# Kernel optimization log

Hardware: AMD Instinct MI355X
Metric: run time of the kernel (lower is better)

## Reference

```python
import jax, jax.numpy as jnp
import numpy as np
import math

B, T, E, H = 4, 1024, 1024, 16
HD = E // H  # 64, even -> rope_dim == head_dim, no pass-through
SCALE = HD ** -0.5
PI = math.pi


def setup_inputs() -> dict:
    key = jax.random.key(0)
    ks = jax.random.split(key, 16)
    d = {}
    d["x_real"] = jax.random.normal(ks[0], (B, T, E), jnp.float32)
    d["x_imag"] = jax.random.normal(ks[1], (B, T, E), jnp.float32)
    d["lat"] = jax.random.uniform(ks[2], (B, T), jnp.float32) * 180.0
    d["lon"] = jax.random.uniform(ks[3], (B, T), jnp.float32) * 360.0
    i = 4
    for p in ("q", "k", "v", "o"):
        d[p + "_log_mag"] = jax.random.normal(ks[i], (E, E), jnp.float32) * 0.1; i += 1
        d[p + "_phase"] = jax.random.uniform(ks[i], (E, E), jnp.float32, minval=-PI, maxval=PI); i += 1
        d[p + "_bmag"] = jnp.zeros((E,), jnp.float32)
        d[p + "_bphase"] = jnp.zeros((E,), jnp.float32)
    d["dist_scale"] = jax.random.normal(ks[i], (H,), jnp.float32) * 0.1 - 0.5; i += 1
    d["dist_offset"] = jnp.zeros((H,), jnp.float32)
    return d


def _clinear(xr, xi, log_mag, phase, bmag, bphase):
    # Complex linear with magnitude-phase weights: W = exp(log_mag) * e^{i*phase}
    mag = jnp.exp(log_mag)
    wr = mag * jnp.cos(phase)
    wi = mag * jnp.sin(phase)
    r = xr @ wr.T - xi @ wi.T + bmag * jnp.cos(bphase)
    im = xr @ wi.T + xi @ wr.T + bmag * jnp.sin(bphase)
    return r, im


def _rotate_half(x):
    x1, x2 = jnp.split(x, 2, axis=-1)
    return jnp.concatenate([-x2, x1], axis=-1)


def _rope(xr, xi, cos_full, sin_full):
    # applied identically to real and imag parts (head_dim even -> full rope)
    r = xr * cos_full + _rotate_half(xr) * sin_full
    im = xi * cos_full + _rotate_half(xi) * sin_full
    return r, im


def _heads(x):  # [B,T,E] -> [B,H,T,HD]
    return x.reshape(B, T, H, HD).transpose(0, 2, 1, 3)


def _forward(x_real, x_imag, lat, lon,
             q_log_mag, q_phase, q_bmag, q_bphase,
             k_log_mag, k_phase, k_bmag, k_bphase,
             v_log_mag, v_phase, v_bmag, v_bphase,
             o_log_mag, o_phase, o_bmag, o_bphase,
             dist_scale, dist_offset):
    qr, qi = _clinear(x_real, x_imag, q_log_mag, q_phase, q_bmag, q_bphase)
    kr, ki = _clinear(x_real, x_imag, k_log_mag, k_phase, k_bmag, k_bphase)
    vr, vi = _clinear(x_real, x_imag, v_log_mag, v_phase, v_bmag, v_bphase)
    qr, qi, kr, ki, vr, vi = map(_heads, (qr, qi, kr, ki, vr, vi))

    # complex RoPE cache
    pos = jnp.arange(T, dtype=jnp.float32)
    inv_freq = 1.0 / (10000.0 ** (jnp.arange(0, HD, 2, dtype=jnp.float32) / HD))
    freqs = pos[:, None] * inv_freq[None, :]          # [T, HD/2]
    cos = jnp.cos(freqs); sin = jnp.sin(freqs)
    cos_full = jnp.concatenate([cos, cos], -1)[None, None]  # [1,1,T,HD]
    sin_full = jnp.concatenate([sin, sin], -1)[None, None]
    qr, qi = _rope(qr, qi, cos_full, sin_full)
    kr, ki = _rope(kr, ki, cos_full, sin_full)

    # Hermitian attention scores: Re(Q K^H) = Re(Q)Re(K)^T + Im(Q)Im(K)^T
    scores = (jnp.einsum('bhqd,bhkd->bhqk', qr, kr)
              + jnp.einsum('bhqd,bhkd->bhqk', qi, ki)) * SCALE

    # spatial attention bias via haversine distance
    lat_rad = (lat - 90.0) / 180.0 * PI
    lon_rad = lon / 360.0 * (2.0 * PI)
    lat1 = lat_rad[:, :, None]; lat2 = lat_rad[:, None, :]   # [B,T,1],[B,1,T]
    dlat = lat2 - lat1
    dlon = lon_rad[:, None, :] - lon_rad[:, :, None]
    a = jnp.sin(dlat / 2) ** 2 + jnp.cos(lat1) * jnp.cos(lat2) * jnp.sin(dlon / 2) ** 2
    dist_deg = 2.0 * jnp.arcsin(jnp.sqrt(jnp.clip(a, 0.0, 1.0))) * (180.0 / PI)
    log_dist = jnp.log1p(dist_deg)[:, None]                  # [B,1,T,T]
    bias = dist_scale[None, :, None, None] * log_dist + dist_offset[None, :, None, None]
    scores = scores + bias

    # causal mask (block_size == T)
    causal = jnp.tril(jnp.ones((T, T), dtype=bool))
    scores = jnp.where(causal[None, None], scores, jnp.float32(-1e9))
    attn = jax.nn.softmax(scores, axis=-1)

    # complex value aggregation: real attention weights times complex V
    or_ = jnp.einsum('bhqk,bhkd->bhqd', attn, vr)
    oi_ = jnp.einsum('bhqk,bhkd->bhqd', attn, vi)
    or_ = or_.transpose(0, 2, 1, 3).reshape(B, T, E)
    oi_ = oi_.transpose(0, 2, 1, 3).reshape(B, T, E)

    yr, yi = _clinear(or_, oi_, o_log_mag, o_phase, o_bmag, o_bphase)
    return jnp.stack([yr, yi])  # [2,B,T,E] (real, imag)


def reference(x_real, x_imag, lat, lon,
              q_log_mag, q_phase, q_bmag, q_bphase,
              k_log_mag, k_phase, k_bmag, k_bphase,
              v_log_mag, v_phase, v_bmag, v_bphase,
              o_log_mag, o_phase, o_bmag, o_bphase,
              dist_scale, dist_offset):
    return _forward(x_real, x_imag, lat, lon,
                    q_log_mag, q_phase, q_bmag, q_bphase,
                    k_log_mag, k_phase, k_bmag, k_bphase,
                    v_log_mag, v_phase, v_bmag, v_bphase,
                    o_log_mag, o_phase, o_bmag, o_bphase,
                    dist_scale, dist_offset)
```

## Files before the change

### kernel.cpp

```cpp
#include <hip/hip_runtime.h>
#include <math.h>

#define B_ 4
#define T_ 1024
#define E_ 1024
#define H_ 16
#define HD_ 64

constexpr float SCALE_ = 0.125f;
constexpr float PI_F = 3.14159265358979323846f;

constexpr size_t BTE = (size_t)B_ * T_ * E_;
constexpr size_t BTT = (size_t)B_ * T_ * T_;
constexpr int M_ = B_ * T_;
constexpr int KC_ = 2 * E_;

typedef __attribute__((ext_vector_type(8))) short bf16x8;
typedef __attribute__((ext_vector_type(4))) float f32x4;

__device__ __forceinline__ short f2bf(float f) {
    unsigned int u = __float_as_uint(f);
    unsigned int r = (u + 0x7fffu + ((u >> 16) & 1u)) >> 16;
    return (short)r;
}
__device__ __forceinline__ float bf2f(short s) {
    return __uint_as_float(((unsigned int)(unsigned short)s) << 16);
}
__device__ __forceinline__ void fsplit(float v, short& h, short& l) {
    short hh = f2bf(v);
    h = hh;
    l = f2bf(v - bf2f(hh));
}
__device__ __forceinline__ void gl_lds16(const void* g, void* l) {
    __builtin_amdgcn_global_load_lds(
        (const __attribute__((address_space(1))) unsigned int*)g,
        (__attribute__((address_space(3))) unsigned int*)l, 16, 0, 0);
}

__global__ __launch_bounds__(256) void wgen(const float* __restrict__ lm,
                                            const float* __restrict__ ph,
                                            short* __restrict__ W) {
    int idx = blockIdx.x * 256 + threadIdx.x;
    int n = idx >> 10, k = idx & 1023;
    float m = expf(lm[idx]);
    float s, c;
    sincosf(ph[idx], &s, &c);
    float wr = m * c, wi = m * s;
    size_t r0 = (size_t)n * KC_;
    size_t r1 = (size_t)(n + 1024) * KC_;
    W[r0 + k]        = f2bf(wr);
    W[r0 + 1024 + k] = f2bf(-wi);
    W[r1 + k]        = f2bf(wi);
    W[r1 + 1024 + k] = f2bf(wr);
}

__global__ __launch_bounds__(256) void wgen_split(const float* __restrict__ lm,
                                                  const float* __restrict__ ph,
                                                  short* __restrict__ Wh,
                                                  short* __restrict__ Wl) {
    int idx = blockIdx.x * 256 + threadIdx.x;
    int n = idx >> 10, k = idx & 1023;
    float m = expf(lm[idx]);
    float s, c;
    sincosf(ph[idx], &s, &c);
    float wr = m * c, wi = m * s;
    size_t o0 = (size_t)n * KC_ + k;
    size_t o1 = (size_t)n * KC_ + 1024 + k;
    size_t o2 = (size_t)(n + 1024) * KC_ + k;
    size_t o3 = (size_t)(n + 1024) * KC_ + 1024 + k;
    short h, l;
    fsplit(wr,  h, l); Wh[o0] = h; Wl[o0] = l;
    fsplit(-wi, h, l); Wh[o1] = h; Wl[o1] = l;
    fsplit(wi,  h, l); Wh[o2] = h; Wl[o2] = l;
    fsplit(wr,  h, l); Wh[o3] = h; Wl[o3] = l;
}

__global__ __launch_bounds__(256) void xcat_split(const float* __restrict__ xr,
                                                  const float* __restrict__ xi,
                                                  short* __restrict__ xh,
                                                  short* __restrict__ xl) {
    size_t idx = (size_t)blockIdx.x * 256 + threadIdx.x;
    size_t m = idx >> 10, k = idx & 1023;
    short h, l;
    fsplit(xr[idx], h, l);
    xh[m * KC_ + k] = h; xl[m * KC_ + k] = l;
    fsplit(xi[idx], h, l);
    xh[m * KC_ + 1024 + k] = h; xl[m * KC_ + 1024 + k] = l;
}

__global__ __launch_bounds__(256) void geodist(const float* __restrict__ lat,
                                               const float* __restrict__ lon,
                                               short* __restrict__ ld) {
    size_t idx = (size_t)blockIdx.x * 256 + threadIdx.x;
    int k = (int)(idx & (T_ - 1));
    int q = (int)((idx >> 10) & (T_ - 1));
    int b = (int)(idx >> 20);
    float la1 = (lat[b * T_ + q] - 90.f) * (PI_F / 180.f);
    float la2 = (lat[b * T_ + k] - 90.f) * (PI_F / 180.f);
    float lo1 = lon[b * T_ + q] * (PI_F / 180.f);
    float lo2 = lon[b * T_ + k] * (PI_F / 180.f);
    float sdla = sinf((la2 - la1) * 0.5f);
    float sdlo = sinf((lo2 - lo1) * 0.5f);
    float a = sdla * sdla + cosf(la1) * cosf(la2) * sdlo * sdlo;
    a = fminf(fmaxf(a, 0.f), 1.f);
    float dd = 2.f * asinf(sqrtf(a)) * (180.f / PI_F);
    ld[idx] = f2bf(log1pf(dd));
}

__global__ __launch_bounds__(512, 2) void cgemm_qk2(const short* __restrict__ Ah,
                                                    const short* __restrict__ Al,
                                                    const short* __restrict__ Qwh,
                                                    const short* __restrict__ Qwl,
                                                    const short* __restrict__ Kwh,
                                                    const short* __restrict__ Kwl,
                                                    const float* __restrict__ qbm,
                                                    const float* __restrict__ qbp,
                                                    const float* __restrict__ kbm,
                                                    const float* __restrict__ kbp,
                                                    short* __restrict__ Qh,
                                                    short* __restrict__ Ql,
                                                    short* __restrict__ Kh,
                                                    short* __restrict__ Kl) {
    __shared__ short lds[2][4096 * 8];

    const int tid = threadIdx.x;
    const int w = tid >> 6, l = tid & 63;
    const int wm = w >> 1;
    const int wn = w & 1;
    const int wl = l & 15, g = l >> 4;

    const int id = blockIdx.x;
    const int x = id & 7;
    const int j = id >> 3;
    const int bm = ((x & 3) * 4 + (j & 3)) * 256;
    const int bnc = ((x >> 2) * 8 + (j >> 2)) * 128;

    f32x4 accQ[4][4], accK[4][4];
#pragma unroll
    for (int m = 0; m < 4; ++m)
#pragma unroll
        for (int n = 0; n < 4; ++n) {
            accQ[m][n] = (f32x4){0.f, 0.f, 0.f, 0.f};
            accK[m][n] = (f32x4){0.f, 0.f, 0.f, 0.f};
        }

    auto stage = [&](int k0, int buf) {
#pragma unroll
        for (int i = 0; i < 8; ++i) {
            const int c = i * 512 + tid;
            short* dst = &lds[buf][(size_t)c * 8];
            if (c < 2048) {
                const int row = c >> 3, c8 = (c & 7) ^ (row & 7);
                gl_lds16(((c8 < 4) ? Ah : Al) + (size_t)(bm + row) * KC_ + k0 + (c8 & 3) * 8, dst);
            } else if (c < 3072) {
                const int lc = c - 2048, row = lc >> 3, c8 = (lc & 7) ^ (row & 7);
                gl_lds16(((c8 < 4) ? Qwh : Qwl) + (size_t)(bnc + row) * KC_ + k0 + (c8 & 3) * 8, dst);
            } else {
                const int lc = c - 3072, row = lc >> 3, c8 = (lc & 7) ^ (row & 7);
                gl_lds16(((c8 < 4) ? Kwh : Kwl) + (size_t)(bnc + row) * KC_ + k0 + (c8 & 3) * 8, dst);
            }
        }
    };

    const int NT = KC_ / 32;
    stage(0, 0);
    __syncthreads();

    int cur = 0;
    for (int t = 0; t < NT; ++t) {
        if (t + 1 < NT) stage((t + 1) * 32, cur ^ 1);

        const short* sA = &lds[cur][0];
        const short* sQ = &lds[cur][2048 * 8];
        const short* sK = &lds[cur][3072 * 8];

        bf16x8 afh[4], afl[4];
#pragma unroll
        for (int m = 0; m < 4; ++m) {
            const int ra = wm * 64 + m * 16 + wl;
            const int sw = ra & 7;
            afh[m] = *(const bf16x8*)&sA[(ra * 8 + (g ^ sw)) * 8];
            afl[m] = *(const bf16x8*)&sA[(ra * 8 + ((g + 4) ^ sw)) * 8];
        }
#pragma unroll
        for (int n = 0; n < 4; ++n) {
            const int rb = wn * 64 + n * 16 + wl;
            const int sw = rb & 7;
            const bf16x8 qh_ = *(const bf16x8*)&sQ[(rb * 8 + (g ^ sw)) * 8];
            const bf16x8 ql_ = *(const bf16x8*)&sQ[(rb * 8 + ((g + 4) ^ sw)) * 8];
            const bf16x8 kh_ = *(const bf16x8*)&sK[(rb * 8 + (g ^ sw)) * 8];
            const bf16x8 kl_ = *(const bf16x8*)&sK[(rb * 8 + ((g + 4) ^ sw)) * 8];
#pragma unroll
            for (int m = 0; m < 4; ++m) {
                accQ[m][n] = __builtin_amdgcn_mfma_f32_16x16x32_bf16(afh[m], qh_, accQ[m][n], 0, 0, 0);
                accQ[m][n] = __builtin_amdgcn_mfma_f32_16x16x32_bf16(afh[m], ql_, accQ[m][n], 0, 0, 0);
                accQ[m][n] = __builtin_amdgcn_mfma_f32_16x16x32_bf16(afl[m], qh_, accQ[m][n], 0, 0, 0);
                accK[m][n] = __builtin_amdgcn_mfma_f32_16x16x32_bf16(afh[m], kh_, accK[m][n], 0, 0, 0);
                accK[m][n] = __builtin_amdgcn_mfma_f32_16x16x32_bf16(afh[m], kl_, accK[m][n], 0, 0, 0);
                accK[m][n] = __builtin_amdgcn_mfma_f32_16x16x32_bf16(afl[m], kh_, accK[m][n], 0, 0, 0);
            }
        }
        __syncthreads();
        cur ^= 1;
    }

#pragma unroll
    for (int n = 0; n < 4; ++n) {
        const int col = bnc + wn * 64 + n * 16 + wl;
        const int ch = col & 1023;
        float qs, qc, ks, kc;
        sincosf(qbp[ch], &qs, &qc);
        sincosf(kbp[ch], &ks, &kc);
        const float qbias = qbm[ch] * (col < 1024 ? qc : qs);
        const float kbias = kbm[ch] * (col < 1024 ? kc : ks);
#pragma unroll
        for (int m = 0; m < 4; ++m)
#pragma unroll
            for (int r = 0; r < 4; ++r) {
                accQ[m][n][r] += qbias;
                accK[m][n][r] += kbias;
            }
    }

#pragma unroll
    for (int n = 0; n < 2; ++n) {
        const int jf = n * 16 + wl;
        const float invf = expf(-(2.f * jf / 64.f) * 9.210340371976184f);
#pragma unroll
        for (int m = 0; m < 4; ++m)
#pragma unroll
            for (int r = 0; r < 4; ++r) {
                const int row = bm + wm * 64 + m * 16 + g * 4 + r;
                const float th = (float)(row & 1023) * invf;
                float s_, c_;
                sincosf(th, &s_, &c_);
                float x1 = accQ[m][n][r], x2 = accQ[m][n + 2][r];
                accQ[m][n][r]     = x1 * c_ - x2 * s_;
                accQ[m][n + 2][r] = x2 * c_ + x1 * s_;
                x1 = accK[m][n][r]; x2 = accK[m][n + 2][r];
                accK[m][n][r]     = x1 * c_ - x2 * s_;
                accK[m][n + 2][r] = x2 * c_ + x1 * s_;
            }
    }

#pragma unroll
    for (int n = 0; n < 4; ++n) {
        const int col = bnc + wn * 64 + n * 16 + wl;
        const int ch = col & 1023;
        const int off = (ch >> 6) * 128 + (ch & 63) + ((col >= 1024) ? 64 : 0);
#pragma unroll
        for (int m = 0; m < 4; ++m)
#pragma unroll
            for (int r = 0; r < 4; ++r) {
                const int row = bm + wm * 64 + m * 16 + g * 4 + r;
                short h_, l_;
                fsplit(accQ[m][n][r], h_, l_);
                Qh[(size_t)row * KC_ + off] = h_;
                Ql[(size_t)row * KC_ + off] = l_;
                fsplit(accK[m][n][r], h_, l_);
                Kh[(size_t)row * KC_ + off] = h_;
                Kl[(size_t)row * KC_ + off] = l_;
            }
    }
}

__global__ __launch_bounds__(256) void cgemm_mfma(const short* __restrict__ A,
                                                  const short* __restrict__ W,
                                                  const float* __restrict__ bmag,
                                                  const float* __restrict__ bphase,
                                                  short* __restrict__ outbf,
                                                  float* __restrict__ outr,
                                                  float* __restrict__ outi,
                                                  int mode) {
    __shared__ short lds[2][1024 * 8];

    const int tid = threadIdx.x;
    const int w = tid >> 6, l = tid & 63;
    const int wm = w >> 1, wn = w & 1;
    const int wl = l & 15, g = l >> 4;

    int id = blockIdx.y * 32 + blockIdx.x;
    int swz = (id & 7) * 64 + (id >> 3);
    const int bm = (swz & 31) * 128;
    const int bn = (swz >> 5) * 128;

    f32x4 acc[4][4];
#pragma unroll
    for (int m = 0; m < 4; ++m)
#pragma unroll
        for (int n = 0; n < 4; ++n) acc[m][n] = (f32x4){0.f, 0.f, 0.f, 0.f};

    auto stage = [&](int k0, int buf) {
#pragma unroll
        for (int i = 0; i < 4; ++i) {
            const int c = i * 256 + tid;
            const int row = c >> 3, c8 = (c & 7) ^ (row & 7);
            const short* src = (c8 < 4)
                ? A + (size_t)(bm + row) * KC_ + k0 + (c8 & 3) * 8
                : W + (size_t)(bn + row) * KC_ + k0 + (c8 & 3) * 8;
            gl_lds16(src, &lds[buf][(size_t)c * 8]);
        }
    };

    const int NT = KC_ / 32;
    stage(0, 0);
    __syncthreads();

    int cur = 0;
    for (int t = 0; t < NT; ++t) {
        if (t + 1 < NT) stage((t + 1) * 32, cur ^ 1);

        const short* sAB = lds[cur];
        bf16x8 af[4], bfr[4];
#pragma unroll
        for (int m = 0; m < 4; ++m) {
            const int ra = wm * 64 + m * 16 + wl;
            af[m] = *(const bf16x8*)&sAB[(ra * 8 + (g ^ (ra & 7))) * 8];
        }
#pragma unroll
        for (int n = 0; n < 4; ++n) {
            const int rb = wn * 64 + n * 16 + wl;
            bfr[n] = *(const bf16x8*)&sAB[(rb * 8 + ((g + 4) ^ (rb & 7))) * 8];
        }
#pragma unroll
        for (int m = 0; m < 4; ++m)
#pragma unroll
            for (int n = 0; n < 4; ++n)
                acc[m][n] = __builtin_amdgcn_mfma_f32_16x16x32_bf16(af[m], bfr[n], acc[m][n], 0, 0, 0);

        __syncthreads();
        cur ^= 1;
    }

#pragma unroll
    for (int n = 0; n < 4; ++n) {
        const int col = bn + wn * 64 + n * 16 + wl;
        const int ch = col & 1023;
        float sb, cb;
        sincosf(bphase[ch], &sb, &cb);
        const float bias = bmag[ch] * (col < 1024 ? cb : sb);
#pragma unroll
        for (int m = 0; m < 4; ++m) {
#pragma unroll
            for (int r = 0; r < 4; ++r) {
                const int row = bm + wm * 64 + m * 16 + g * 4 + r;
                const float v = acc[m][n][r] + bias;
                if (mode == 0) {
                    const int hh = ch >> 6, d = ch & 63;
                    outbf[(size_t)row * KC_ + hh * 128 + d + ((col >= 1024) ? 64 : 0)] = f2bf(v);
                } else {
                    if (col < 1024) outr[(size_t)row * E_ + col] = v;
                    else            outi[(size_t)row * E_ + (col - 1024)] = v;
                }
            }
        }
    }
}

__global__ __launch_bounds__(512) void attn_split(const short* __restrict__ qh,
                                                  const short* __restrict__ ql,
                                                  const short* __restrict__ kh,
                                                  const short* __restrict__ kl,
                                                  const short* __restrict__ vc,
                                                  const short* __restrict__ ldb,
                                                  const float* __restrict__ dsc,
                                                  const float* __restrict__ dof,
                                                  short* __restrict__ otc) {
    __shared__ short sKh[64 * 128];
    __shared__ short sKl[64 * 128];
    __shared__ short sV[2][64 * 66];
    __shared__ short sP[8][16 * 68];

    const int j = blockIdx.x;
    const int h = j & 15;
    const int idx = j >> 4;
    const int b = idx & 3;
    const int q4 = idx >> 2;
    const int qt = (q4 < 4) ? (7 - q4) : (q4 - 4);

    const int tid = threadIdx.x;
    const int w = tid >> 6, l = tid & 63;
    const int wl = l & 15, g = l >> 4;

    const float dsch = dsc[h], dofh = dof[h];

    bf16x8 aqh[4], aql[4];
    {
        const size_t qbase = ((size_t)(b * T_) + qt * 128 + w * 16 + wl) * KC_ + h * 128;
#pragma unroll
        for (int ks = 0; ks < 4; ++ks) {
            aqh[ks] = *(const bf16x8*)(qh + qbase + ks * 32 + g * 8);
            aql[ks] = *(const bf16x8*)(ql + qbase + ks * 32 + g * 8);
        }
    }

    f32x4 accR[4], accI[4];
#pragma unroll
    for (int nb = 0; nb < 4; ++nb) {
        accR[nb] = (f32x4){0.f, 0.f, 0.f, 0.f};
        accI[nb] = (f32x4){0.f, 0.f, 0.f, 0.f};
    }
    float m_run[4], l_run[4];
#pragma unroll
    for (int r = 0; r < 4; ++r) { m_run[r] = -3.0e38f; l_run[r] = 0.f; }

    const int nkt = 2 * qt + 2;
    for (int kt = 0; kt < nkt; ++kt) {
        __syncthreads();

#pragma unroll
        for (int i = 0; i < 2; ++i) {
            int chunk = (w * 2 + i) * 64 + l;
            int row = chunk >> 4;
            int c8 = (chunk & 15) ^ (row & 15);
            size_t src = ((size_t)(b * T_) + kt * 64 + row) * KC_ + h * 128 + c8 * 8;
            gl_lds16(kh + src, sKh + (w * 2 + i) * 64 * 8);
            gl_lds16(kl + src, sKl + (w * 2 + i) * 64 * 8);
        }
        {
            const short* vrow = vc + ((size_t)(b * T_) + kt * 64 + l) * KC_ + h * 128;
            const int comp = w >> 2;
            const int d0 = (w & 3) * 16;
#pragma unroll
            for (int half = 0; half < 2; ++half) {
                bf16x8 v8 = *(const bf16x8*)(vrow + comp * 64 + d0 + half * 8);
#pragma unroll
                for (int jj = 0; jj < 8; ++jj) sV[comp][(d0 + half * 8 + jj) * 66 + l] = v8[jj];
            }
        }
        __syncthreads();

        f32x4 s[4];
#pragma unroll
        for (int nb = 0; nb < 4; ++nb) s[nb] = (f32x4){0.f, 0.f, 0.f, 0.f};
#pragma unroll
        for (int nb = 0; nb < 4; ++nb) {
            const int ktl = nb * 16 + wl;
#pragma unroll
            for (int ks = 0; ks < 4; ++ks) {
                const int pc8 = (ks * 4 + g) ^ (ktl & 15);
                const bf16x8 bkh = *(const bf16x8*)&sKh[ktl * 128 + pc8 * 8];
                const bf16x8 bkl = *(const bf16x8*)&sKl[ktl * 128 + pc8 * 8];
                s[nb] = __builtin_amdgcn_mfma_f32_16x16x32_bf16(aqh[ks], bkh, s[nb], 0, 0, 0);
                s[nb] = __builtin_amdgcn_mfma_f32_16x16x32_bf16(aqh[ks], bkl, s[nb], 0, 0, 0);
                s[nb] = __builtin_amdgcn_mfma_f32_16x16x32_bf16(aql[ks], bkh, s[nb], 0, 0, 0);
            }
        }

        const int qg0 = qt * 128 + w * 16 + g * 4;
        const int kg0 = kt * 64;
        const bool domask = (kt >= 2 * qt);
#pragma unroll
        for (int nb = 0; nb < 4; ++nb) {
            const int kg = kg0 + nb * 16 + wl;
            const short* ldp = ldb + ((size_t)b * T_ + qg0) * T_ + kg;
#pragma unroll
            for (int r = 0; r < 4; ++r) {
                float sv = s[nb][r] * SCALE_ + dsch * bf2f(ldp[(size_t)r * T_]) + dofh;
                if (domask && kg > qg0 + r) sv = -1.0e9f;
                s[nb][r] = sv;
            }
        }

#pragma unroll
        for (int r = 0; r < 4; ++r) {
            float mt = fmaxf(fmaxf(s[0][r], s[1][r]), fmaxf(s[2][r], s[3][r]));
            mt = fmaxf(mt, __shfl_xor(mt, 1));
            mt = fmaxf(mt, __shfl_xor(mt, 2));
            mt = fmaxf(mt, __shfl_xor(mt, 4));
            mt = fmaxf(mt, __shfl_xor(mt, 8));
            const float mnew = fmaxf(m_run[r], mt);
            const float sc = __expf(m_run[r] - mnew);
            m_run[r] = mnew;
            float rs = 0.f;
#pragma unroll
            for (int nb = 0; nb < 4; ++nb) {
                const float p = __expf(s[nb][r] - mnew);
                s[nb][r] = p;
                rs += p;
            }
            rs += __shfl_xor(rs, 1);
            rs += __shfl_xor(rs, 2);
            rs += __shfl_xor(rs, 4);
            rs += __shfl_xor(rs, 8);
            l_run[r] = l_run[r] * sc + rs;
#pragma unroll
            for (int nb = 0; nb < 4; ++nb) { accR[nb][r] *= sc; accI[nb][r] *= sc; }
        }

#pragma unroll
        for (int nb = 0; nb < 4; ++nb)
#pragma unroll
            for (int r = 0; r < 4; ++r)
                sP[w][(g * 4 + r) * 68 + nb * 16 + wl] = f2bf(s[nb][r]);

        bf16x8 ap[2];
#pragma unroll
        for (int ks = 0; ks < 2; ++ks)
            ap[ks] = *(const bf16x8*)&sP[w][wl * 68 + ks * 32 + g * 8];
#pragma unroll
        for (int nb = 0; nb < 4; ++nb) {
#pragma unroll
            for (int ks = 0; ks < 2; ++ks) {
                const bf16x8 bvr = *(const bf16x8*)&sV[0][(nb * 16 + wl) * 66 + ks * 32 + g * 8];
                const bf16x8 bvi = *(const bf16x8*)&sV[1][(nb * 16 + wl) * 66 + ks * 32 + g * 8];
                accR[nb] = __builtin_amdgcn_mfma_f32_16x16x32_bf16(ap[ks], bvr, accR[nb], 0, 0, 0);
                accI[nb] = __builtin_amdgcn_mfma_f32_16x16x32_bf16(ap[ks], bvi, accI[nb], 0, 0, 0);
            }
        }
    }

    float inv[4];
#pragma unroll
    for (int r = 0; r < 4; ++r) inv[r] = 1.0f / l_run[r];
#pragma unroll
    for (int nb = 0; nb < 4; ++nb) {
#pragma unroll
        for (int r = 0; r < 4; ++r) {
            const int q = qt * 128 + w * 16 + g * 4 + r;
            const int d = nb * 16 + wl;
            const size_t base = ((size_t)(b * T_) + q) * KC_ + h * 64 + d;
            otc[base] = f2bf(accR[nb][r] * inv[r]);
            otc[base + 1024] = f2bf(accI[nb][r] * inv[r]);
        }
    }
}

extern "C" void kernel_launch(void* const* d_in, const int* in_sizes, int n_in,
                              void* d_out, int out_size, void* d_ws, size_t ws_size,
                              hipStream_t stream) {
    const float* x_r  = (const float*)d_in[0];
    const float* x_i  = (const float*)d_in[1];
    const float* lat  = (const float*)d_in[2];
    const float* lon  = (const float*)d_in[3];
    const float* q_lm = (const float*)d_in[4];
    const float* q_ph = (const float*)d_in[5];
    const float* q_bm = (const float*)d_in[6];
    const float* q_bp = (const float*)d_in[7];
    const float* k_lm = (const float*)d_in[8];
    const float* k_ph = (const float*)d_in[9];
    const float* k_bm = (const float*)d_in[10];
    const float* k_bp = (const float*)d_in[11];
    const float* v_lm = (const float*)d_in[12];
    const float* v_ph = (const float*)d_in[13];
    const float* v_bm = (const float*)d_in[14];
    const float* v_bp = (const float*)d_in[15];
    const float* o_lm = (const float*)d_in[16];
    const float* o_ph = (const float*)d_in[17];
    const float* o_bm = (const float*)d_in[18];
    const float* o_bp = (const float*)d_in[19];
    const float* dsc  = (const float*)d_in[20];
    const float* dof  = (const float*)d_in[21];

    char* ws = (char*)d_ws;
    const size_t MB = 1024u * 1024u;
    short* Wv  = (short*)(ws + 0 * MB);
    short* Wo  = (short*)(ws + 8 * MB);
    short* Wqh = (short*)(ws + 16 * MB);
    short* Wql = (short*)(ws + 24 * MB);
    short* Wkh = (short*)(ws + 32 * MB);
    short* Wkl = (short*)(ws + 40 * MB);
    short* xch = (short*)(ws + 48 * MB);
    short* xcl = (short*)(ws + 64 * MB);
    short* qhh = (short*)(ws + 80 * MB);
    short* qll = (short*)(ws + 96 * MB);
    short* khh = (short*)(ws + 112 * MB);
    short* kll = (short*)(ws + 128 * MB);
    short* vcb = (short*)(ws + 144 * MB);
    short* otc = (short*)(ws + 160 * MB);
    short* ldt = (short*)(ws + 176 * MB);

    wgen_split<<<(E_ * E_) / 256, 256, 0, stream>>>(q_lm, q_ph, Wqh, Wql);
    wgen_split<<<(E_ * E_) / 256, 256, 0, stream>>>(k_lm, k_ph, Wkh, Wkl);
    wgen<<<(E_ * E_) / 256, 256, 0, stream>>>(v_lm, v_ph, Wv);
    wgen<<<(E_ * E_) / 256, 256, 0, stream>>>(o_lm, o_ph, Wo);
    xcat_split<<<BTE / 256, 256, 0, stream>>>(x_r, x_i, xch, xcl);
    geodist<<<BTT / 256, 256, 0, stream>>>(lat, lon, ldt);

    cgemm_qk2<<<256, 512, 0, stream>>>(xch, xcl, Wqh, Wql, Wkh, Wkl,
                                       q_bm, q_bp, k_bm, k_bp,
                                       qhh, qll, khh, kll);

    dim3 ggrid(M_ / 128, KC_ / 128);
    cgemm_mfma<<<ggrid, 256, 0, stream>>>(xch, Wv, v_bm, v_bp, vcb, nullptr, nullptr, 0);

    attn_split<<<512, 512, 0, stream>>>(qhh, qll, khh, kll, vcb, ldt, dsc, dof, otc);

    float* yr = (float*)d_out;
    float* yi = (float*)d_out + BTE;
    cgemm_mfma<<<ggrid, 256, 0, stream>>>(otc, Wo, o_bm, o_bp, nullptr, yr, yi, 1);
}
```

Measured before the change: 603.6 us.

## Deepen GEMM LDS pipeline to two tiles in flight with explicit vmcnt waits

Both GEMM kernels now keep two K-tiles in flight. They replace __syncthreads with raw s_barrier plus explicit s_waitcnt vmcnt/lgkmcnt counts, and load all LDS fragments into registers before a second barrier. The next-next tile is then issued into the just-consumed buffer before the MFMA block runs. This is meant to hide global-to-LDS latency behind compute and avoid the full vmcnt(0) drain that __syncthreads implies. The cost is more fragment registers, and correctness depends on the hardcoded vmcnt counts matching the number of loads each stage issues.

```diff
diff --git a/kernel.cpp b/kernel.cpp
--- a/kernel.cpp
+++ b/kernel.cpp
@@ -35,6 +35,11 @@
     __builtin_amdgcn_global_load_lds(
         (const __attribute__((address_space(1))) unsigned int*)g,
         (__attribute__((address_space(3))) unsigned int*)l, 16, 0, 0);
+}
+__device__ __forceinline__ void barrier_raw() {
+    asm volatile("" ::: "memory");
+    __builtin_amdgcn_s_barrier();
+    asm volatile("" ::: "memory");
 }
 
 __global__ __launch_bounds__(256) void wgen(const float* __restrict__ lm,
@@ -164,17 +169,20 @@
 
     const int NT = KC_ / 32;
     stage(0, 0);
-    __syncthreads();
+    stage(32, 1);
 
     int cur = 0;
     for (int t = 0; t < NT; ++t) {
-        if (t + 1 < NT) stage((t + 1) * 32, cur ^ 1);
+        if (t == NT - 1) asm volatile("s_waitcnt vmcnt(0)" ::: "memory");
+        else             asm volatile("s_waitcnt vmcnt(8)" ::: "memory");
+        __builtin_amdgcn_sched_barrier(0);
+        barrier_raw();
 
         const short* sA = &lds[cur][0];
         const short* sQ = &lds[cur][2048 * 8];
         const short* sK = &lds[cur][3072 * 8];
 
-        bf16x8 afh[4], afl[4];
+        bf16x8 afh[4], afl[4], qh_[4], ql_[4], kh_[4], kl_[4];
 #pragma unroll
         for (int m = 0; m < 4; ++m) {
             const int ra = wm * 64 + m * 16 + wl;
@@ -186,21 +194,29 @@
         for (int n = 0; n < 4; ++n) {
             const int rb = wn * 64 + n * 16 + wl;
             const int sw = rb & 7;
-            const bf16x8 qh_ = *(const bf16x8*)&sQ[(rb * 8 + (g ^ sw)) * 8];
-            const bf16x8 ql_ = *(const bf16x8*)&sQ[(rb * 8 + ((g + 4) ^ sw)) * 8];
-            const bf16x8 kh_ = *(const bf16x8*)&sK[(rb * 8 + (g ^ sw)) * 8];
-            const bf16x8 kl_ = *(const bf16x8*)&sK[(rb * 8 + ((g + 4) ^ sw)) * 8];
+            qh_[n] = *(const bf16x8*)&sQ[(rb * 8 + (g ^ sw)) * 8];
+            ql_[n] = *(const bf16x8*)&sQ[(rb * 8 + ((g + 4) ^ sw)) * 8];
+            kh_[n] = *(const bf16x8*)&sK[(rb * 8 + (g ^ sw)) * 8];
+            kl_[n] = *(const bf16x8*)&sK[(rb * 8 + ((g + 4) ^ sw)) * 8];
+        }
+        asm volatile("s_waitcnt lgkmcnt(0)" ::: "memory");
+        __builtin_amdgcn_sched_barrier(0);
+        barrier_raw();
+
+        if (t + 2 < NT) stage((t + 2) * 32, cur);
+
+#pragma unroll
+        for (int n = 0; n < 4; ++n) {
 #pragma unroll
             for (int m = 0; m < 4; ++m) {
-                accQ[m][n] = __builtin_amdgcn_mfma_f32_16x16x32_bf16(afh[m], qh_, accQ[m][n], 0, 0, 0);
-                accQ[m][n] = __builtin_amdgcn_mfma_f32_16x16x32_bf16(afh[m], ql_, accQ[m][n], 0, 0, 0);
-                accQ[m][n] = __builtin_amdgcn_mfma_f32_16x16x32_bf16(afl[m], qh_, accQ[m][n], 0, 0, 0);
-                accK[m][n] = __builtin_amdgcn_mfma_f32_16x16x32_bf16(afh[m], kh_, accK[m][n], 0, 0, 0);
-                accK[m][n] = __builtin_amdgcn_mfma_f32_16x16x32_bf16(afh[m], kl_, accK[m][n], 0, 0, 0);
-                accK[m][n] = __builtin_amdgcn_mfma_f32_16x16x32_bf16(afl[m], kh_, accK[m][n], 0, 0, 0);
-            }
-        }
-        __syncthreads();
+                accQ[m][n] = __builtin_amdgcn_mfma_f32_16x16x32_bf16(afh[m], qh_[n], accQ[m][n], 0, 0, 0);
+                accQ[m][n] = __builtin_amdgcn_mfma_f32_16x16x32_bf16(afh[m], ql_[n], accQ[m][n], 0, 0, 0);
+                accQ[m][n] = __builtin_amdgcn_mfma_f32_16x16x32_bf16(afl[m], qh_[n], accQ[m][n], 0, 0, 0);
+                accK[m][n] = __builtin_amdgcn_mfma_f32_16x16x32_bf16(afh[m], kh_[n], accK[m][n], 0, 0, 0);
+                accK[m][n] = __builtin_amdgcn_mfma_f32_16x16x32_bf16(afh[m], kl_[n], accK[m][n], 0, 0, 0);
+                accK[m][n] = __builtin_amdgcn_mfma_f32_16x16x32_bf16(afl[m], kh_[n], accK[m][n], 0, 0, 0);
+            }
+        }
         cur ^= 1;
     }
 
@@ -304,11 +320,14 @@
 
     const int NT = KC_ / 32;
     stage(0, 0);
-    __syncthreads();
+    stage(32, 1);
 
     int cur = 0;
     for (int t = 0; t < NT; ++t) {
-        if (t + 1 < NT) stage((t + 1) * 32, cur ^ 1);
+        if (t == NT - 1) asm volatile("s_waitcnt vmcnt(0)" ::: "memory");
+        else             asm volatile("s_waitcnt vmcnt(4)" ::: "memory");
+        __builtin_amdgcn_sched_barrier(0);
+        barrier_raw();
 
         const short* sAB = lds[cur];
         bf16x8 af[4], bfr[4];
@@ -322,13 +341,18 @@
             const int rb = wn * 64 + n * 16 + wl;
             bfr[n] = *(const bf16x8*)&sAB[(rb * 8 + ((g + 4) ^ (rb & 7))) * 8];
         }
+        asm volatile("s_waitcnt lgkmcnt(0)" ::: "memory");
+        __builtin_amdgcn_sched_barrier(0);
+        barrier_raw();
+
+        if (t + 2 < NT) stage((t + 2) * 32, cur);
+
 #pragma unroll
         for (int m = 0; m < 4; ++m)
 #pragma unroll
             for (int n = 0; n < 4; ++n)
                 acc[m][n] = __builtin_amdgcn_mfma_f32_16x16x32_bf16(af[m], bfr[n], acc[m][n], 0, 0, 0);
 
-        __syncthreads();
         cur ^= 1;
     }
 
```

Result: slower. 834.7 us (+38.3%).

## Load QK GEMM A-operand directly to registers and shrink tile to 128 rows

Applied to the files above, without the earlier changes.

The fused Q/K projection GEMM now uses 256-thread blocks with a 128x128 output tile, launched as 512 blocks instead of 256. Activation (A) fragments are prefetched straight from global memory into registers one k-step ahead, so only the Q and K weight tiles are staged through LDS. This halves LDS usage and spreads work over more blocks, at the cost of more register pressure for the prefetched fragments and uncoalesced, unshared global reads of A.

```diff
diff --git a/kernel.cpp b/kernel.cpp
--- a/kernel.cpp
+++ b/kernel.cpp
@@ -107,7 +107,7 @@
     ld[idx] = f2bf(log1pf(dd));
 }
 
-__global__ __launch_bounds__(512, 2) void cgemm_qk2(const short* __restrict__ Ah,
+__global__ __launch_bounds__(256, 2) void cgemm_qk2(const short* __restrict__ Ah,
                                                     const short* __restrict__ Al,
                                                     const short* __restrict__ Qwh,
                                                     const short* __restrict__ Qwl,
@@ -121,7 +121,7 @@
                                                     short* __restrict__ Ql,
                                                     short* __restrict__ Kh,
                                                     short* __restrict__ Kl) {
-    __shared__ short lds[2][4096 * 8];
+    __shared__ short lds[2][2048 * 8];
 
     const int tid = threadIdx.x;
     const int w = tid >> 6, l = tid & 63;
@@ -132,8 +132,8 @@
     const int id = blockIdx.x;
     const int x = id & 7;
     const int j = id >> 3;
-    const int bm = ((x & 3) * 4 + (j & 3)) * 256;
-    const int bnc = ((x >> 2) * 8 + (j >> 2)) * 128;
+    const int bm = ((x & 3) * 8 + (j & 7)) * 128;
+    const int bn = ((x >> 2) * 8 + (j >> 3)) * 128;
 
     f32x4 accQ[4][4], accK[4][4];
 #pragma unroll
@@ -144,69 +144,78 @@
             accK[m][n] = (f32x4){0.f, 0.f, 0.f, 0.f};
         }
 
+    bf16x8 aCh[4], aCl[4], aNh[4], aNl[4];
+    auto loadA = [&](int k0, bf16x8* hd, bf16x8* ld_) {
+#pragma unroll
+        for (int m = 0; m < 4; ++m) {
+            const size_t ar = (size_t)(bm + wm * 64 + m * 16 + wl) * KC_ + k0 + g * 8;
+            hd[m] = *(const bf16x8*)(Ah + ar);
+            ld_[m] = *(const bf16x8*)(Al + ar);
+        }
+    };
+
     auto stage = [&](int k0, int buf) {
 #pragma unroll
         for (int i = 0; i < 8; ++i) {
-            const int c = i * 512 + tid;
+            const int c = i * 256 + tid;
             short* dst = &lds[buf][(size_t)c * 8];
-            if (c < 2048) {
+            if (c < 1024) {
                 const int row = c >> 3, c8 = (c & 7) ^ (row & 7);
-                gl_lds16(((c8 < 4) ? Ah : Al) + (size_t)(bm + row) * KC_ + k0 + (c8 & 3) * 8, dst);
-            } else if (c < 3072) {
-                const int lc = c - 2048, row = lc >> 3, c8 = (lc & 7) ^ (row & 7);
-                gl_lds16(((c8 < 4) ? Qwh : Qwl) + (size_t)(bnc + row) * KC_ + k0 + (c8 & 3) * 8, dst);
+                gl_lds16(((c8 < 4) ? Qwh : Qwl) + (size_t)(bn + row) * KC_ + k0 + (c8 & 3) * 8, dst);
             } else {
-                const int lc = c - 3072, row = lc >> 3, c8 = (lc & 7) ^ (row & 7);
-                gl_lds16(((c8 < 4) ? Kwh : Kwl) + (size_t)(bnc + row) * KC_ + k0 + (c8 & 3) * 8, dst);
+                const int lc = c - 1024, row = lc >> 3, c8 = (lc & 7) ^ (row & 7);
+                gl_lds16(((c8 < 4) ? Kwh : Kwl) + (size_t)(bn + row) * KC_ + k0 + (c8 & 3) * 8, dst);
             }
         }
     };
 
     const int NT = KC_ / 32;
+    loadA(0, aCh, aCl);
     stage(0, 0);
     __syncthreads();
 
     int cur = 0;
     for (int t = 0; t < NT; ++t) {
-        if (t + 1 < NT) stage((t + 1) * 32, cur ^ 1);
-
-        const short* sA = &lds[cur][0];
-        const short* sQ = &lds[cur][2048 * 8];
-        const short* sK = &lds[cur][3072 * 8];
-
-        bf16x8 afh[4], afl[4];
-#pragma unroll
-        for (int m = 0; m < 4; ++m) {
-            const int ra = wm * 64 + m * 16 + wl;
-            const int sw = ra & 7;
-            afh[m] = *(const bf16x8*)&sA[(ra * 8 + (g ^ sw)) * 8];
-            afl[m] = *(const bf16x8*)&sA[(ra * 8 + ((g + 4) ^ sw)) * 8];
-        }
+        if (t + 1 < NT) {
+            loadA((t + 1) * 32, aNh, aNl);
+            stage((t + 1) * 32, cur ^ 1);
+        }
+
+        const short* sQ = &lds[cur][0];
+        const short* sK = &lds[cur][1024 * 8];
+
+        bf16x8 qh_[4], ql_[4], kh_[4], kl_[4];
 #pragma unroll
         for (int n = 0; n < 4; ++n) {
             const int rb = wn * 64 + n * 16 + wl;
             const int sw = rb & 7;
-            const bf16x8 qh_ = *(const bf16x8*)&sQ[(rb * 8 + (g ^ sw)) * 8];
-            const bf16x8 ql_ = *(const bf16x8*)&sQ[(rb * 8 + ((g + 4) ^ sw)) * 8];
-            const bf16x8 kh_ = *(const bf16x8*)&sK[(rb * 8 + (g ^ sw)) * 8];
-            const bf16x8 kl_ = *(const bf16x8*)&sK[(rb * 8 + ((g + 4) ^ sw)) * 8];
+            qh_[n] = *(const bf16x8*)&sQ[(rb * 8 + (g ^ sw)) * 8];
+            ql_[n] = *(const bf16x8*)&sQ[(rb * 8 + ((g + 4) ^ sw)) * 8];
+            kh_[n] = *(const bf16x8*)&sK[(rb * 8 + (g ^ sw)) * 8];
+            kl_[n] = *(const bf16x8*)&sK[(rb * 8 + ((g + 4) ^ sw)) * 8];
+        }
+
+#pragma unroll
+        for (int n = 0; n < 4; ++n) {
 #pragma unroll
             for (int m = 0; m < 4; ++m) {
-                accQ[m][n] = __builtin_amdgcn_mfma_f32_16x16x32_bf16(afh[m], qh_, accQ[m][n], 0, 0, 0);
-                accQ[m][n] = __builtin_amdgcn_mfma_f32_16x16x32_bf16(afh[m], ql_, accQ[m][n], 0, 0, 0);
-                accQ[m][n] = __builtin_amdgcn_mfma_f32_16x16x32_bf16(afl[m], qh_, accQ[m][n], 0, 0, 0);
-                accK[m][n] = __builtin_amdgcn_mfma_f32_16x16x32_bf16(afh[m], kh_, accK[m][n], 0, 0, 0);
-                accK[m][n] = __builtin_amdgcn_mfma_f32_16x16x32_bf16(afh[m], kl_, accK[m][n], 0, 0, 0);
-                accK[m][n] = __builtin_amdgcn_mfma_f32_16x16x32_bf16(afl[m], kh_, accK[m][n], 0, 0, 0);
+                accQ[m][n] = __builtin_amdgcn_mfma_f32_16x16x32_bf16(aCh[m], qh_[n], accQ[m][n], 0, 0, 0);
+                accQ[m][n] = __builtin_amdgcn_mfma_f32_16x16x32_bf16(aCh[m], ql_[n], accQ[m][n], 0, 0, 0);
+                accQ[m][n] = __builtin_amdgcn_mfma_f32_16x16x32_bf16(aCl[m], qh_[n], accQ[m][n], 0, 0, 0);
+                accK[m][n] = __builtin_amdgcn_mfma_f32_16x16x32_bf16(aCh[m], kh_[n], accK[m][n], 0, 0, 0);
+                accK[m][n] = __builtin_amdgcn_mfma_f32_16x16x32_bf16(aCh[m], kl_[n], accK[m][n], 0, 0, 0);
+                accK[m][n] = __builtin_amdgcn_mfma_f32_16x16x32_bf16(aCl[m], kh_[n], accK[m][n], 0, 0, 0);
             }
         }
         __syncthreads();
         cur ^= 1;
+#pragma unroll
+        for (int m = 0; m < 4; ++m) { aCh[m] = aNh[m]; aCl[m] = aNl[m]; }
     }
 
 #pragma unroll
     for (int n = 0; n < 4; ++n) {
-        const int col = bnc + wn * 64 + n * 16 + wl;
+        const int col = bn + wn * 64 + n * 16 + wl;
         const int ch = col & 1023;
         float qs, qc, ks, kc;
         sincosf(qbp[ch], &qs, &qc);
@@ -245,7 +254,7 @@
 
 #pragma unroll
     for (int n = 0; n < 4; ++n) {
-        const int col = bnc + wn * 64 + n * 16 + wl;
+        const int col = bn + wn * 64 + n * 16 + wl;
         const int ch = col & 1023;
         const int off = (ch >> 6) * 128 + (ch & 63) + ((col >= 1024) ? 64 : 0);
 #pragma unroll
@@ -577,7 +586,7 @@
     xcat_split<<<BTE / 256, 256, 0, stream>>>(x_r, x_i, xch, xcl);
     geodist<<<BTT / 256, 256, 0, stream>>>(lat, lon, ldt);
 
-    cgemm_qk2<<<256, 512, 0, stream>>>(xch, xcl, Wqh, Wql, Wkh, Wkl,
+    cgemm_qk2<<<512, 256, 0, stream>>>(xch, xcl, Wqh, Wql, Wkh, Wkl,
                                        q_bm, q_bp, k_bm, k_bp,
                                        qhh, qll, khh, kll);
 
```

Result: slower. 673.5 us (+11.6%).

## Split fused Q/K projection GEMM into separate smaller-tile blocks

Applied to the files above, without the earlier changes.

Replaces the fused Q+K GEMM kernel (512 threads, 256x128 tile, A tile shared by both Q and K weights) with a 256-thread kernel where each block computes either Q or K on a 128x128 tile, launching 1024 blocks instead of 256. This lowers per-block registers and LDS, aiming for better occupancy and more even load across CUs. The cost is that each A tile is now loaded twice (once for Q, once for K), which raises global and LDS traffic.

```diff
diff --git a/kernel.cpp b/kernel.cpp
--- a/kernel.cpp
+++ b/kernel.cpp
@@ -107,57 +107,55 @@
     ld[idx] = f2bf(log1pf(dd));
 }
 
-__global__ __launch_bounds__(512, 2) void cgemm_qk2(const short* __restrict__ Ah,
-                                                    const short* __restrict__ Al,
-                                                    const short* __restrict__ Qwh,
-                                                    const short* __restrict__ Qwl,
-                                                    const short* __restrict__ Kwh,
-                                                    const short* __restrict__ Kwl,
-                                                    const float* __restrict__ qbm,
-                                                    const float* __restrict__ qbp,
-                                                    const float* __restrict__ kbm,
-                                                    const float* __restrict__ kbp,
-                                                    short* __restrict__ Qh,
-                                                    short* __restrict__ Ql,
-                                                    short* __restrict__ Kh,
-                                                    short* __restrict__ Kl) {
-    __shared__ short lds[2][4096 * 8];
+__global__ __launch_bounds__(256, 2) void cgemm_qk_split(const short* __restrict__ Ah,
+                                                         const short* __restrict__ Al,
+                                                         const short* __restrict__ Qwh,
+                                                         const short* __restrict__ Qwl,
+                                                         const short* __restrict__ Kwh,
+                                                         const short* __restrict__ Kwl,
+                                                         const float* __restrict__ qbm,
+                                                         const float* __restrict__ qbp,
+                                                         const float* __restrict__ kbm,
+                                                         const float* __restrict__ kbp,
+                                                         short* __restrict__ Qh,
+                                                         short* __restrict__ Ql,
+                                                         short* __restrict__ Kh,
+                                                         short* __restrict__ Kl) {
+    __shared__ short lds[2][2048 * 8];
 
     const int tid = threadIdx.x;
     const int w = tid >> 6, l = tid & 63;
-    const int wm = w >> 1;
-    const int wn = w & 1;
+    const int wm = w >> 1, wn = w & 1;
     const int wl = l & 15, g = l >> 4;
 
     const int id = blockIdx.x;
-    const int x = id & 7;
-    const int j = id >> 3;
-    const int bm = ((x & 3) * 4 + (j & 3)) * 256;
-    const int bnc = ((x >> 2) * 8 + (j >> 2)) * 128;
-
-    f32x4 accQ[4][4], accK[4][4];
+    const int sel = id >> 9;
+    const int p = id & 511;
+    const int x = p & 7;
+    const int jj = p >> 3;
+    const int bm = ((x & 3) * 8 + (jj & 7)) * 128;
+    const int bn = ((x >> 2) * 8 + (jj >> 3)) * 128;
+
+    const short* Wh = sel ? Kwh : Qwh;
+    const short* Wl2 = sel ? Kwl : Qwl;
+
+    f32x4 acc[4][4];
 #pragma unroll
     for (int m = 0; m < 4; ++m)
 #pragma unroll
-        for (int n = 0; n < 4; ++n) {
-            accQ[m][n] = (f32x4){0.f, 0.f, 0.f, 0.f};
-            accK[m][n] = (f32x4){0.f, 0.f, 0.f, 0.f};
-        }
+        for (int n = 0; n < 4; ++n) acc[m][n] = (f32x4){0.f, 0.f, 0.f, 0.f};
 
     auto stage = [&](int k0, int buf) {
 #pragma unroll
         for (int i = 0; i < 8; ++i) {
-            const int c = i * 512 + tid;
+            const int c = i * 256 + tid;
             short* dst = &lds[buf][(size_t)c * 8];
-            if (c < 2048) {
+            if (c < 1024) {
                 const int row = c >> 3, c8 = (c & 7) ^ (row & 7);
                 gl_lds16(((c8 < 4) ? Ah : Al) + (size_t)(bm + row) * KC_ + k0 + (c8 & 3) * 8, dst);
-            } else if (c < 3072) {
-                const int lc = c - 2048, row = lc >> 3, c8 = (lc & 7) ^ (row & 7);
-                gl_lds16(((c8 < 4) ? Qwh : Qwl) + (size_t)(bnc + row) * KC_ + k0 + (c8 & 3) * 8, dst);
             } else {
-                const int lc = c - 3072, row = lc >> 3, c8 = (lc & 7) ^ (row & 7);
-                gl_lds16(((c8 < 4) ? Kwh : Kwl) + (size_t)(bnc + row) * KC_ + k0 + (c8 & 3) * 8, dst);
+                const int lc = c - 1024, row = lc >> 3, c8 = (lc & 7) ^ (row & 7);
+                gl_lds16(((c8 < 4) ? Wh : Wl2) + (size_t)(bn + row) * KC_ + k0 + (c8 & 3) * 8, dst);
             }
         }
     };
@@ -171,10 +169,9 @@
         if (t + 1 < NT) stage((t + 1) * 32, cur ^ 1);
 
         const short* sA = &lds[cur][0];
-        const short* sQ = &lds[cur][2048 * 8];
-        const short* sK = &lds[cur][3072 * 8];
-
-        bf16x8 afh[4], afl[4];
+        const short* sW = &lds[cur][1024 * 8];
+
+        bf16x8 afh[4], afl[4], wfh[4], wfl[4];
 #pragma unroll
         for (int m = 0; m < 4; ++m) {
             const int ra = wm * 64 + m * 16 + wl;
@@ -186,40 +183,38 @@
         for (int n = 0; n < 4; ++n) {
             const int rb = wn * 64 + n * 16 + wl;
             const int sw = rb & 7;
-            const bf16x8 qh_ = *(const bf16x8*)&sQ[(rb * 8 + (g ^ sw)) * 8];
-            const bf16x8 ql_ = *(const bf16x8*)&sQ[(rb * 8 + ((g + 4) ^ sw)) * 8];
-            const bf16x8 kh_ = *(const bf16x8*)&sK[(rb * 8 + (g ^ sw)) * 8];
-            const bf16x8 kl_ = *(const bf16x8*)&sK[(rb * 8 + ((g + 4) ^ sw)) * 8];
+            wfh[n] = *(const bf16x8*)&sW[(rb * 8 + (g ^ sw)) * 8];
+            wfl[n] = *(const bf16x8*)&sW[(rb * 8 + ((g + 4) ^ sw)) * 8];
+        }
+#pragma unroll
+        for (int n = 0; n < 4; ++n)
 #pragma unroll
             for (int m = 0; m < 4; ++m) {
-                accQ[m][n] = __builtin_amdgcn_mfma_f32_16x16x32_bf16(afh[m], qh_, accQ[m][n], 0, 0, 0);
-                accQ[m][n] = __builtin_amdgcn_mfma_f32_16x16x32_bf16(afh[m], ql_, accQ[m][n], 0, 0, 0);
-                accQ[m][n] = __builtin_amdgcn_mfma_f32_16x16x32_bf16(afl[m], qh_, accQ[m][n], 0, 0, 0);
-                accK[m][n] = __builtin_amdgcn_mfma_f32_16x16x32_bf16(afh[m], kh_, accK[m][n], 0, 0, 0);
-                accK[m][n] = __builtin_amdgcn_mfma_f32_16x16x32_bf16(afh[m], kl_, accK[m][n], 0, 0, 0);
-                accK[m][n] = __builtin_amdgcn_mfma_f32_16x16x32_bf16(afl[m], kh_, accK[m][n], 0, 0, 0);
-            }
-        }
+                acc[m][n] = __builtin_amdgcn_mfma_f32_16x16x32_bf16(afh[m], wfh[n], acc[m][n], 0, 0, 0);
+                acc[m][n] = __builtin_amdgcn_mfma_f32_16x16x32_bf16(afh[m], wfl[n], acc[m][n], 0, 0, 0);
+                acc[m][n] = __builtin_amdgcn_mfma_f32_16x16x32_bf16(afl[m], wfh[n], acc[m][n], 0, 0, 0);
+            }
+
         __syncthreads();
         cur ^= 1;
     }
 
+    const float* bmag = sel ? kbm : qbm;
+    const float* bphs = sel ? kbp : qbp;
+    short* Oh = sel ? Kh : Qh;
+    short* Ol = sel ? Kl : Ql;
+
 #pragma unroll
     for (int n = 0; n < 4; ++n) {
-        const int col = bnc + wn * 64 + n * 16 + wl;
+        const int col = bn + wn * 64 + n * 16 + wl;
         const int ch = col & 1023;
-        float qs, qc, ks, kc;
-        sincosf(qbp[ch], &qs, &qc);
-        sincosf(kbp[ch], &ks, &kc);
-        const float qbias = qbm[ch] * (col < 1024 ? qc : qs);
-        const float kbias = kbm[ch] * (col < 1024 ? kc : ks);
+        float sb, cb;
+        sincosf(bphs[ch], &sb, &cb);
+        const float bias = bmag[ch] * (col < 1024 ? cb : sb);
 #pragma unroll
         for (int m = 0; m < 4; ++m)
 #pragma unroll
-            for (int r = 0; r < 4; ++r) {
-                accQ[m][n][r] += qbias;
-                accK[m][n][r] += kbias;
-            }
+            for (int r = 0; r < 4; ++r) acc[m][n][r] += bias;
     }
 
 #pragma unroll
@@ -234,18 +229,15 @@
                 const float th = (float)(row & 1023) * invf;
                 float s_, c_;
                 sincosf(th, &s_, &c_);
-                float x1 = accQ[m][n][r], x2 = accQ[m][n + 2][r];
-                accQ[m][n][r]     = x1 * c_ - x2 * s_;
-                accQ[m][n + 2][r] = x2 * c_ + x1 * s_;
-                x1 = accK[m][n][r]; x2 = accK[m][n + 2][r];
-                accK[m][n][r]     = x1 * c_ - x2 * s_;
-                accK[m][n + 2][r] = x2 * c_ + x1 * s_;
+                const float x1 = acc[m][n][r], x2 = acc[m][n + 2][r];
+                acc[m][n][r]     = x1 * c_ - x2 * s_;
+                acc[m][n + 2][r] = x2 * c_ + x1 * s_;
             }
     }
 
 #pragma unroll
     for (int n = 0; n < 4; ++n) {
-        const int col = bnc + wn * 64 + n * 16 + wl;
+        const int col = bn + wn * 64 + n * 16 + wl;
         const int ch = col & 1023;
         const int off = (ch >> 6) * 128 + (ch & 63) + ((col >= 1024) ? 64 : 0);
 #pragma unroll
@@ -254,12 +246,9 @@
             for (int r = 0; r < 4; ++r) {
                 const int row = bm + wm * 64 + m * 16 + g * 4 + r;
                 short h_, l_;
-                fsplit(accQ[m][n][r], h_, l_);
-                Qh[(size_t)row * KC_ + off] = h_;
-                Ql[(size_t)row * KC_ + off] = l_;
-                fsplit(accK[m][n][r], h_, l_);
-                Kh[(size_t)row * KC_ + off] = h_;
-                Kl[(size_t)row * KC_ + off] = l_;
+                fsplit(acc[m][n][r], h_, l_);
+                Oh[(size_t)row * KC_ + off] = h_;
+                Ol[(size_t)row * KC_ + off] = l_;
             }
     }
 }
@@ -577,9 +566,9 @@
     xcat_split<<<BTE / 256, 256, 0, stream>>>(x_r, x_i, xch, xcl);
     geodist<<<BTT / 256, 256, 0, stream>>>(lat, lon, ldt);
 
-    cgemm_qk2<<<256, 512, 0, stream>>>(xch, xcl, Wqh, Wql, Wkh, Wkl,
-                                       q_bm, q_bp, k_bm, k_bp,
-                                       qhh, qll, khh, kll);
+    cgemm_qk_split<<<1024, 256, 0, stream>>>(xch, xcl, Wqh, Wql, Wkh, Wkl,
+                                             q_bm, q_bp, k_bm, k_bp,
+                                             qhh, qll, khh, kll);
 
     dim3 ggrid(M_ / 128, KC_ / 128);
     cgemm_mfma<<<ggrid, 256, 0, stream>>>(xch, Wv, v_bm, v_bp, vcb, nullptr, nullptr, 0);
```

New measurement: 727.4 us. 1.21x slower.
